# Kernel tuning notes

Hardware: AMD Instinct MI355X
Metric: run time of the kernel (lower is better)

Reference implementation:

```python
import jax, jax.numpy as jnp
import numpy as np

K = 3          # deformable kernel size
N = K * K      # sampling points per output pixel
PAD = 1
BN_EPS = 1e-5


def setup_inputs() -> dict:
    key = jax.random.key(0)
    ks = jax.random.split(key, 6)
    B, C, H, W = 32, 103, 32, 32
    Cout = 32
    x = jax.random.normal(ks[0], (B, C, H, W), jnp.float32)
    # offset-predicting conv: 2*N output channels (N y-offsets then N x-offsets)
    w_off = jax.random.normal(ks[1], (2 * N, C, K, K), jnp.float32) * 0.01
    b_off = jnp.zeros((2 * N,), jnp.float32)
    # main deformable conv weight
    w = jax.random.normal(ks[2], (Cout, C, K, K), jnp.float32) * (1.0 / np.sqrt(C * N))
    b = jnp.zeros((Cout,), jnp.float32)
    # BatchNorm (eval mode) params
    gamma = jax.random.uniform(ks[3], (Cout,), jnp.float32, 0.5, 1.5)
    beta = jax.random.normal(ks[4], (Cout,), jnp.float32) * 0.1
    run_mean = jax.random.normal(ks[5], (Cout,), jnp.float32) * 0.1
    run_var = jnp.ones((Cout,), jnp.float32)
    return {"x": x, "w_off": w_off, "b_off": b_off, "w": w, "b": b,
            "gamma": gamma, "beta": beta, "run_mean": run_mean, "run_var": run_var}


def _deform_conv(x, w_off, b_off, w, b):
    B, C, H, W = x.shape
    # predicted offsets: (B, 2N, H, W) -> (B, H, W, N) each for y and x
    off = jax.lax.conv_general_dilated(x, w_off, (1, 1), [(PAD, PAD), (PAD, PAD)])
    off = off + b_off[None, :, None, None]
    off_y = jnp.transpose(off[:, :N], (0, 2, 3, 1))
    off_x = jnp.transpose(off[:, N:], (0, 2, 3, 1))
    # regular kernel grid offsets p_n in {-1,0,1}^2
    ky, kx = jnp.meshgrid(jnp.arange(-1, 2, dtype=jnp.float32),
                          jnp.arange(-1, 2, dtype=jnp.float32), indexing='ij')
    kn_y, kn_x = ky.reshape(-1), kx.reshape(-1)  # (N,)
    # base grid p_0 in padded coordinates (stride 1, padding 1 -> starts at 1)
    p0_y = jnp.arange(1, H + 1, dtype=jnp.float32)[None, :, None, None]
    p0_x = jnp.arange(1, W + 1, dtype=jnp.float32)[None, None, :, None]
    Hp, Wp = H + 2 * PAD, W + 2 * PAD
    py = jnp.clip(p0_y + kn_y + off_y, 0.0, Hp - 1.0)  # (B,H,W,N)
    px = jnp.clip(p0_x + kn_x + off_x, 0.0, Wp - 1.0)
    # zero-padded input, flattened spatial for gather
    xp = jnp.pad(x, ((0, 0), (0, 0), (PAD, PAD), (PAD, PAD)))
    xf = xp.reshape(B, C, Hp * Wp)
    y0 = jnp.clip(jnp.floor(py).astype(jnp.int32), 0, Hp - 2)
    x0 = jnp.clip(jnp.floor(px).astype(jnp.int32), 0, Wp - 2)
    y1, x1 = y0 + 1, x0 + 1
    wy = (py - y0.astype(py.dtype))[:, None]  # (B,1,H,W,N)
    wx = (px - x0.astype(px.dtype))[:, None]

    def gather(yi, xi):
        idx = (yi * Wp + xi).reshape(B, -1)                      # (B, H*W*N)
        g = jnp.take_along_axis(xf, idx[:, None, :], axis=2)    # (B, C, H*W*N)
        return g.reshape(B, C, H, W, N)

    v00, v01 = gather(y0, x0), gather(y0, x1)
    v10, v11 = gather(y1, x0), gather(y1, x1)
    samp = (v00 * (1 - wy) * (1 - wx) + v01 * (1 - wy) * wx
            + v10 * wy * (1 - wx) + v11 * wy * wx)               # (B,C,H,W,N)
    out = jnp.einsum('bchwn,ocn->bohw', samp, w.reshape(w.shape[0], C, N))
    return out + b[None, :, None, None]


def reference(x, w_off, b_off, w, b, gamma, beta, run_mean, run_var):
    out = _deform_conv(x, w_off, b_off, w, b)
    # BatchNorm2d (eval mode) + ReLU
    inv = gamma * jax.lax.rsqrt(run_var + BN_EPS)
    out = out * inv[None, :, None, None] + (beta - run_mean * inv)[None, :, None, None]
    return jax.nn.relu(out)
```

## Files before the change

### kernel.cpp

```cpp
#include <hip/hip_runtime.h>


#define CC    103
#define COUT  32
#define KSC   5
#define RSU   34
#define PLSU  1164
#define NPAIR 8
#define BUF_U (NPAIR * PLSU)

typedef __attribute__((ext_vector_type(8))) _Float16 f16x8;
typedef __attribute__((ext_vector_type(2))) _Float16 h2;
typedef __attribute__((ext_vector_type(2))) __fp16  fp16x2;
typedef __attribute__((ext_vector_type(4))) float f32x4;

#define WTPM_W 0
#define WTPO_W 17920
#define BN_W   35840

__global__ void k_prep(const float* __restrict__ w, const float* __restrict__ w_off,
                       const float* __restrict__ bias, const float* __restrict__ gamma,
                       const float* __restrict__ beta, const float* __restrict__ mean,
                       const float* __restrict__ var,
                       unsigned short* __restrict__ wtpm, unsigned short* __restrict__ wtpo,
                       float* __restrict__ bn) {
    int tid = blockIdx.x * 256 + threadIdx.x;
    if (tid < 71680) {
        int half_ = tid >= 35840 ? 1 : 0;
        int e = tid - half_ * 35840;
        const float* src = half_ ? w_off : w;
        unsigned short* dst = half_ ? wtpo : wtpm;
        int mrows = half_ ? 18 : 32;
        int j = e & 7, lane = (e >> 3) & 63, tile = e >> 9;
        int mt = tile & 1, chs = tile >> 1;
        int s = chs % 5, ch = chs / 5;
        int o = mt * 16 + (lane & 15);
        int kl = s * 32 + (lane >> 4) * 8 + j;
        int n = kl >> 4, c = ch * 16 + (kl & 15);
        float v = 0.f;
        if (n < 9 && c < CC && o < mrows) v = src[o * (CC * 9) + c * 9 + n];
        union { _Float16 h; unsigned short u; } cv;
        cv.h = (_Float16)v;
        dst[e] = cv.u;
    }
    if (tid < 32) {
        float inv = gamma[tid] * rsqrtf(var[tid] + 1e-5f);
        bn[tid]      = inv;
        bn[32 + tid] = beta[tid] + (bias[tid] - mean[tid]) * inv;
    }
}

__global__ void __launch_bounds__(512, 4)
k_fused(const float* __restrict__ x, const float* __restrict__ b_off,
        const unsigned short* __restrict__ wtpo, const unsigned short* __restrict__ wtpm,
        const float* __restrict__ bn, float* __restrict__ out) {
    __shared__ unsigned int ldsp[2 * BUF_U];
    __shared__ float exch[18 * 64];

    int bid = blockIdx.x;
    int b   = (bid & 7) * 4 + ((bid >> 3) & 3);
    int pxg = bid >> 5;

    int t = threadIdx.x, lane = t & 63, wv = t >> 6;
    int kh = wv >> 2;
    int pxl = (wv & 3) * 16 + (lane & 15);
    int px  = pxg * 64 + pxl;
    int h = px >> 5, wq = px & 31;
    int kg = lane >> 4;
    int hi = kg >> 1;
    int pb = (kg & 1) * 4;

    unsigned int* mybuf = ldsp + kh * BUF_U;

    const float* xb = x + b * (CC * 1024);
    int tl = t & 255;
    int sr = tl >> 3, sk = (tl & 7) * 4;

    int r0 = 2 * pxg - 1; if (r0 < 0) r0 = 0;
    int r1 = 2 * pxg + 2; if (r1 > 31) r1 = 31;
    bool rowact = (sr >= r0 && sr <= r1);

    const int KYL[5] = {0,0,1,2,2}, KXL[5] = {0,2,1,0,2};
    const int KYH[5] = {0,1,1,2,2}, KXH[5] = {1,0,2,1,2};
    const int TAPL[5] = {0,2,4,6,8}, TAPH[5] = {1,3,5,7,8};
    int myky[5], mykx[5], mytap[5];
#pragma unroll
    for (int s = 0; s < 5; s++) {
        myky[s] = hi ? KYH[s] : KYL[s];
        mykx[s] = hi ? KXH[s] : KXL[s];
        mytap[s] = hi ? TAPH[s] : TAPL[s];
    }

    float4 L[NPAIR], M[NPAIR];
    auto loadx = [&](int ch, bool full) {
        if (!full && !rowact) return;
        const float* s0 = xb + sr * 32 + sk;
#pragma unroll
        for (int i = 0; i < NPAIR; i++) {
            int c = ch * 16 + 2 * i;
            if (c < CC) {
                L[i] = *(const float4*)(s0 + c * 1024);
                if (c + 1 < CC) M[i] = *(const float4*)(s0 + (c + 1) * 1024);
                else            M[i] = make_float4(0.f, 0.f, 0.f, 0.f);
            }
        }
    };
    auto packwrite = [&](int ch, bool full) {
        if (!full && !rowact) return;
        unsigned int* dstb = mybuf + (sr + 1) * RSU + 2 + sk;
#pragma unroll
        for (int i = 0; i < NPAIR; i++) {
            int c = ch * 16 + 2 * i;
            if (c < CC) {
                union { fp16x2 hh; unsigned u; } p0, p1, p2, p3;
                p0.hh = __builtin_amdgcn_cvt_pkrtz(L[i].x, M[i].x);
                p1.hh = __builtin_amdgcn_cvt_pkrtz(L[i].y, M[i].y);
                p2.hh = __builtin_amdgcn_cvt_pkrtz(L[i].z, M[i].z);
                p3.hh = __builtin_amdgcn_cvt_pkrtz(L[i].w, M[i].w);
                *(uint2*)(dstb + i * PLSU)     = make_uint2(p0.u, p1.u);
                *(uint2*)(dstb + i * PLSU + 2) = make_uint2(p2.u, p3.u);
            }
        }
    };

    auto chunk1 = [&](int it) { return kh ? (2 * it) : (it < 3 ? 2 * it + 1 : -1); };
    auto chunk2 = [&](int it) { return kh ? (6 - 2 * it) : (it < 3 ? 5 - 2 * it : -1); };
    int fullIt = 2 + kh;

    f32x4 acc0 = {0.f, 0.f, 0.f, 0.f};
    f32x4 acc1 = {0.f, 0.f, 0.f, 0.f};

    loadx(chunk1(0), false);
    for (int i = t; i < 2 * BUF_U; i += 512) ldsp[i] = 0u;
    __syncthreads();

    for (int it = 0; it < 4; it++) {
        int ch = chunk1(it);
        if (ch >= 0) packwrite(ch, it == fullIt);
        __syncthreads();
        int nx = (it < 3) ? chunk1(it + 1) : -1;
        if (nx >= 0) loadx(nx, it + 1 == fullIt);
        if (ch >= 0) {
            const unsigned short* wch = wtpo + ch * 5120;
#pragma unroll
            for (int s = 0; s < KSC; s++) {
                const unsigned int* cell = mybuf + pb * PLSU
                    + (h + myky[s]) * RSU + 1 + (wq + mykx[s]);
                union { unsigned u[4]; f16x8 v; } bu;
#pragma unroll
                for (int jj = 0; jj < 4; jj++) bu.u[jj] = cell[jj * PLSU];
                f16x8 a0 = *(const f16x8*)(wch + s * 1024 + lane * 8);
                f16x8 a1 = *(const f16x8*)(wch + s * 1024 + 512 + lane * 8);
                acc0 = __builtin_amdgcn_mfma_f32_16x16x32_f16(a0, bu.v, acc0, 0, 0, 0);
                acc1 = __builtin_amdgcn_mfma_f32_16x16x32_f16(a1, bu.v, acc1, 0, 0, 0);
            }
        }
        __syncthreads();
    }

    if (kh == 0) {
        float* ex = exch + pxl;
#pragma unroll
        for (int reg = 0; reg < 4; reg++) ex[(kg * 4 + reg) * 64] = acc0[reg];
        if (kg == 0) { ex[16 * 64] = acc1[0]; ex[17 * 64] = acc1[1]; }
    }
    __syncthreads();
    if (kh == 1) {
        float* ex = exch + pxl;
#pragma unroll
        for (int reg = 0; reg < 4; reg++) ex[(kg * 4 + reg) * 64] += acc0[reg];
        if (kg == 0) { ex[16 * 64] += acc1[0]; ex[17 * 64] += acc1[1]; }
    }
    __syncthreads();

    int cofs[KSC];
    h2  W[KSC][4];
#pragma unroll
    for (int s = 0; s < KSC; s++) {
        int tap = mytap[s];
        float oy = exch[tap * 64 + pxl] + b_off[tap];
        float ox = exch[(9 + tap) * 64 + pxl] + b_off[9 + tap];
        float py  = (float)(h + myky[s]) + oy;
        float pxx = (float)(wq + mykx[s]) + ox;
        py  = fminf(fmaxf(py, 0.f), 33.f);
        pxx = fminf(fmaxf(pxx, 0.f), 33.f);
        int y0 = min((int)py, 32);
        int x0 = min((int)pxx, 32);
        float fy = py - (float)y0;
        float fx = pxx - (float)x0;
        float w00 = (1.f - fy) * (1.f - fx), w01 = (1.f - fy) * fx;
        float w10 = fy * (1.f - fx),          w11 = fy * fx;
        W[s][0] = (h2){(_Float16)w00, (_Float16)w00};
        W[s][1] = (h2){(_Float16)w01, (_Float16)w01};
        W[s][2] = (h2){(_Float16)w10, (_Float16)w10};
        W[s][3] = (h2){(_Float16)w11, (_Float16)w11};
        cofs[s] = pb * PLSU + y0 * RSU + 1 + x0;
    }

    acc0 = (f32x4){0.f, 0.f, 0.f, 0.f};
    acc1 = (f32x4){0.f, 0.f, 0.f, 0.f};
    for (int it = 0; it < 4; it++) {
        int ch = chunk2(it);
        if (it > 0) {
            if (ch >= 0) packwrite(ch, true);
            else {
                float* e = (float*)ldsp + pxl;
#pragma unroll
                for (int reg = 0; reg < 4; reg++) {
                    e[(kg * 4 + reg) * 64]      = acc0[reg];
                    e[(16 + kg * 4 + reg) * 64] = acc1[reg];
                }
            }
        }
        __syncthreads();
        int nx = (it < 3) ? chunk2(it + 1) : -1;
        if (nx >= 0) loadx(nx, true);
        if (ch >= 0) {
            const unsigned short* wch = wtpm + ch * 5120;
#pragma unroll
            for (int s = 0; s < KSC; s++) {
                const unsigned int* cell = mybuf + cofs[s];
                union { unsigned u[4]; f16x8 v; } bu;
#pragma unroll
                for (int jj = 0; jj < 4; jj++) {
                    union { unsigned u; h2 hh; } t0, t1, b0, b1;
                    t0.u = cell[jj * PLSU];
                    t1.u = cell[jj * PLSU + 1];
                    b0.u = cell[jj * PLSU + RSU];
                    b1.u = cell[jj * PLSU + RSU + 1];
                    h2 sm = t0.hh * W[s][0] + t1.hh * W[s][1]
                          + b0.hh * W[s][2] + b1.hh * W[s][3];
                    union { h2 hh; unsigned u; } r; r.hh = sm;
                    bu.u[jj] = r.u;
                }
                f16x8 a0 = *(const f16x8*)(wch + s * 1024 + lane * 8);
                f16x8 a1 = *(const f16x8*)(wch + s * 1024 + 512 + lane * 8);
                acc0 = __builtin_amdgcn_mfma_f32_16x16x32_f16(a0, bu.v, acc0, 0, 0, 0);
                acc1 = __builtin_amdgcn_mfma_f32_16x16x32_f16(a1, bu.v, acc1, 0, 0, 0);
            }
        }
        __syncthreads();
    }

    if (kh == 1) {
        const float* ex2 = (const float*)ldsp;
        float* op = out + (size_t)b * COUT * 1024 + px;
#pragma unroll
        for (int mt = 0; mt < 2; mt++) {
            f32x4 a = mt ? acc1 : acc0;
#pragma unroll
            for (int reg = 0; reg < 4; reg++) {
                int o = mt * 16 + kg * 4 + reg;
                float tot = a[reg] + ex2[o * 64 + pxl];
                float v = tot * bn[o] + bn[32 + o];
                op[o * 1024] = fmaxf(v, 0.f);
            }
        }
    }
}

extern "C" void kernel_launch(void* const* d_in, const int* in_sizes, int n_in,
                              void* d_out, int out_size, void* d_ws, size_t ws_size,
                              hipStream_t stream) {
    const float* x      = (const float*)d_in[0];
    const float* w_off  = (const float*)d_in[1];
    const float* b_off  = (const float*)d_in[2];
    const float* w      = (const float*)d_in[3];
    const float* bias   = (const float*)d_in[4];
    const float* gamma  = (const float*)d_in[5];
    const float* beta   = (const float*)d_in[6];
    const float* rmean  = (const float*)d_in[7];
    const float* rvar   = (const float*)d_in[8];
    float* out = (float*)d_out;

    float* ws = (float*)d_ws;
    unsigned short* wtpm = (unsigned short*)(ws + WTPM_W);
    unsigned short* wtpo = (unsigned short*)(ws + WTPO_W);
    float*          bn   = ws + BN_W;

    k_prep <<<280, 256, 0, stream>>>(w, w_off, bias, gamma, beta, rmean, rvar,
                                     wtpm, wtpo, bn);
    k_fused<<<512, 512, 0, stream>>>(x, b_off, wtpo, wtpm, bn, out);
}
```

Measured before the change: 103.2 us.

## Pre-pack input to fp16 channel pairs in prep kernel; zero only LDS halo

The prep kernel gains extra blocks that convert x to fp16 and interleave channel pairs into a workspace buffer. The fused kernel then loads those packed words and writes them straight to LDS, with no per-tile conversion. This halves the global bytes each fused block reads, because every block rereads its batch's rows. LDS zero-initialisation now touches only the halo border cells instead of the whole buffer. The cost is an extra full pass over x plus a write and reread of the packed copy, and the prep kernel does more work.

```diff
diff --git a/kernel.cpp b/kernel.cpp
--- a/kernel.cpp
+++ b/kernel.cpp
@@ -17,41 +17,66 @@
 #define WTPM_W 0
 #define WTPO_W 17920
 #define BN_W   35840
-
-__global__ void k_prep(const float* __restrict__ w, const float* __restrict__ w_off,
+#define XPK_W  35904
+
+__global__ void k_prep(const float* __restrict__ x,
+                       const float* __restrict__ w, const float* __restrict__ w_off,
                        const float* __restrict__ bias, const float* __restrict__ gamma,
                        const float* __restrict__ beta, const float* __restrict__ mean,
                        const float* __restrict__ var,
                        unsigned short* __restrict__ wtpm, unsigned short* __restrict__ wtpo,
-                       float* __restrict__ bn) {
-    int tid = blockIdx.x * 256 + threadIdx.x;
-    if (tid < 71680) {
-        int half_ = tid >= 35840 ? 1 : 0;
-        int e = tid - half_ * 35840;
-        const float* src = half_ ? w_off : w;
-        unsigned short* dst = half_ ? wtpo : wtpm;
-        int mrows = half_ ? 18 : 32;
-        int j = e & 7, lane = (e >> 3) & 63, tile = e >> 9;
-        int mt = tile & 1, chs = tile >> 1;
-        int s = chs % 5, ch = chs / 5;
-        int o = mt * 16 + (lane & 15);
-        int kl = s * 32 + (lane >> 4) * 8 + j;
-        int n = kl >> 4, c = ch * 16 + (kl & 15);
-        float v = 0.f;
-        if (n < 9 && c < CC && o < mrows) v = src[o * (CC * 9) + c * 9 + n];
-        union { _Float16 h; unsigned short u; } cv;
-        cv.h = (_Float16)v;
-        dst[e] = cv.u;
-    }
-    if (tid < 32) {
-        float inv = gamma[tid] * rsqrtf(var[tid] + 1e-5f);
-        bn[tid]      = inv;
-        bn[32 + tid] = beta[tid] + (bias[tid] - mean[tid]) * inv;
+                       float* __restrict__ bn, unsigned int* __restrict__ xpk) {
+    int bx = blockIdx.x;
+    if (bx < 280) {
+        int tid = bx * 256 + threadIdx.x;
+        if (tid < 71680) {
+            int half_ = tid >= 35840 ? 1 : 0;
+            int e = tid - half_ * 35840;
+            const float* src = half_ ? w_off : w;
+            unsigned short* dst = half_ ? wtpo : wtpm;
+            int mrows = half_ ? 18 : 32;
+            int j = e & 7, lane = (e >> 3) & 63, tile = e >> 9;
+            int mt = tile & 1, chs = tile >> 1;
+            int s = chs % 5, ch = chs / 5;
+            int o = mt * 16 + (lane & 15);
+            int kl = s * 32 + (lane >> 4) * 8 + j;
+            int n = kl >> 4, c = ch * 16 + (kl & 15);
+            float v = 0.f;
+            if (n < 9 && c < CC && o < mrows) v = src[o * (CC * 9) + c * 9 + n];
+            union { _Float16 h; unsigned short u; } cv;
+            cv.h = (_Float16)v;
+            dst[e] = cv.u;
+        }
+        if (tid < 32) {
+            float inv = gamma[tid] * rsqrtf(var[tid] + 1e-5f);
+            bn[tid]      = inv;
+            bn[32 + tid] = beta[tid] + (bias[tid] - mean[tid]) * inv;
+        }
+    } else {
+        int pb = bx - 280;
+        int b = pb / 7, ch = pb - b * 7;
+        int tl = threadIdx.x;
+        const float* xb = x + b * (CC * 1024) + tl * 4;
+        unsigned int* dst = xpk + pb * 8192 + tl * 4;
+#pragma unroll
+        for (int i = 0; i < NPAIR; i++) {
+            int c = ch * 16 + 2 * i;
+            float4 L = make_float4(0.f, 0.f, 0.f, 0.f);
+            float4 M = make_float4(0.f, 0.f, 0.f, 0.f);
+            if (c < CC)     L = *(const float4*)(xb + c * 1024);
+            if (c + 1 < CC) M = *(const float4*)(xb + (c + 1) * 1024);
+            union { fp16x2 hh; unsigned u; } p0, p1, p2, p3;
+            p0.hh = __builtin_amdgcn_cvt_pkrtz(L.x, M.x);
+            p1.hh = __builtin_amdgcn_cvt_pkrtz(L.y, M.y);
+            p2.hh = __builtin_amdgcn_cvt_pkrtz(L.z, M.z);
+            p3.hh = __builtin_amdgcn_cvt_pkrtz(L.w, M.w);
+            *(uint4*)(dst + i * 1024) = make_uint4(p0.u, p1.u, p2.u, p3.u);
+        }
     }
 }
 
 __global__ void __launch_bounds__(512, 4)
-k_fused(const float* __restrict__ x, const float* __restrict__ b_off,
+k_fused(const unsigned int* __restrict__ xpk, const float* __restrict__ b_off,
         const unsigned short* __restrict__ wtpo, const unsigned short* __restrict__ wtpm,
         const float* __restrict__ bn, float* __restrict__ out) {
     __shared__ unsigned int ldsp[2 * BUF_U];
@@ -72,7 +97,6 @@
 
     unsigned int* mybuf = ldsp + kh * BUF_U;
 
-    const float* xb = x + b * (CC * 1024);
     int tl = t & 255;
     int sr = tl >> 3, sk = (tl & 7) * 4;
 
@@ -91,35 +115,20 @@
         mytap[s] = hi ? TAPH[s] : TAPL[s];
     }
 
-    float4 L[NPAIR], M[NPAIR];
+    uint4 U[NPAIR];
     auto loadx = [&](int ch, bool full) {
         if (!full && !rowact) return;
-        const float* s0 = xb + sr * 32 + sk;
-#pragma unroll
-        for (int i = 0; i < NPAIR; i++) {
-            int c = ch * 16 + 2 * i;
-            if (c < CC) {
-                L[i] = *(const float4*)(s0 + c * 1024);
-                if (c + 1 < CC) M[i] = *(const float4*)(s0 + (c + 1) * 1024);
-                else            M[i] = make_float4(0.f, 0.f, 0.f, 0.f);
-            }
-        }
+        const unsigned int* s0 = xpk + (b * 7 + ch) * 8192 + tl * 4;
+#pragma unroll
+        for (int i = 0; i < NPAIR; i++) U[i] = *(const uint4*)(s0 + i * 1024);
     };
     auto packwrite = [&](int ch, bool full) {
         if (!full && !rowact) return;
         unsigned int* dstb = mybuf + (sr + 1) * RSU + 2 + sk;
 #pragma unroll
         for (int i = 0; i < NPAIR; i++) {
-            int c = ch * 16 + 2 * i;
-            if (c < CC) {
-                union { fp16x2 hh; unsigned u; } p0, p1, p2, p3;
-                p0.hh = __builtin_amdgcn_cvt_pkrtz(L[i].x, M[i].x);
-                p1.hh = __builtin_amdgcn_cvt_pkrtz(L[i].y, M[i].y);
-                p2.hh = __builtin_amdgcn_cvt_pkrtz(L[i].z, M[i].z);
-                p3.hh = __builtin_amdgcn_cvt_pkrtz(L[i].w, M[i].w);
-                *(uint2*)(dstb + i * PLSU)     = make_uint2(p0.u, p1.u);
-                *(uint2*)(dstb + i * PLSU + 2) = make_uint2(p2.u, p3.u);
-            }
+            *(uint2*)(dstb + i * PLSU)     = make_uint2(U[i].x, U[i].y);
+            *(uint2*)(dstb + i * PLSU + 2) = make_uint2(U[i].z, U[i].w);
         }
     };
 
@@ -131,7 +140,14 @@
     f32x4 acc1 = {0.f, 0.f, 0.f, 0.f};
 
     loadx(chunk1(0), false);
-    for (int i = t; i < 2 * BUF_U; i += 512) ldsp[i] = 0u;
+    for (int i = t; i < 2240; i += 512) {
+        int plane = i / 140, r = i - plane * 140;
+        int off;
+        if (r < 34)      off = r;
+        else if (r < 76) off = 1122 + (r - 34);
+        else { int rr = (r - 76) >> 1; off = (rr + 1) * 34 + ((r - 76) & 1); }
+        ldsp[(plane >> 3) * BUF_U + (plane & 7) * PLSU + off] = 0u;
+    }
     __syncthreads();
 
     for (int it = 0; it < 4; it++) {
@@ -277,8 +293,9 @@
     unsigned short* wtpm = (unsigned short*)(ws + WTPM_W);
     unsigned short* wtpo = (unsigned short*)(ws + WTPO_W);
     float*          bn   = ws + BN_W;
-
-    k_prep <<<280, 256, 0, stream>>>(w, w_off, bias, gamma, beta, rmean, rvar,
-                                     wtpm, wtpo, bn);
-    k_fused<<<512, 512, 0, stream>>>(x, b_off, wtpo, wtpm, bn, out);
+    unsigned int*   xpk  = (unsigned int*)(ws + XPK_W);
+
+    k_prep <<<504, 256, 0, stream>>>(x, w, w_off, bias, gamma, beta, rmean, rvar,
+                                     wtpm, wtpo, bn, xpk);
+    k_fused<<<512, 512, 0, stream>>>(xpk, b_off, wtpo, wtpm, bn, out);
 }
```

Result: no change. 103.8 us (+0.5%).
